# Optimization experiments

Measured on AMD Instinct MI355X. Metric: run time of the kernel, lower is better.

## Reference

```python
import jax, jax.numpy as jnp
import numpy as np

EBIT = 8
BITS = 8  # wl_activate


def block_quantize_global(data, bits):
    """SWALP block quantize, scalar/global path (small_block='None', dim<=4).

    max-abs reduce -> floor(log2) exponent, clamped to signed ebit range ->
    scale -> round-to-nearest-even -> clamp to signed `bits` range -> rescale.
    If max-abs is exactly 0, data is returned unchanged.
    """
    max_entry = jnp.max(jnp.abs(data))
    # guard log2(0); result unused when max_entry == 0
    safe_max = jnp.where(max_entry == 0, jnp.float32(1.0), max_entry)
    max_exponent = jnp.floor(jnp.log2(safe_max))
    emin = -(2.0 ** (EBIT - 1))
    emax = 2.0 ** (EBIT - 1) - 1
    max_exponent = jnp.clip(max_exponent, emin, emax)
    scale = jnp.exp2(-max_exponent + (bits - 2))
    i = jnp.round(data * scale)  # torch.round_ and jnp.round both round half-to-even
    qmin = -(2.0 ** (bits - 1))
    qmax = 2.0 ** (bits - 1) - 1
    i = jnp.clip(i, qmin, qmax)
    out = i * jnp.exp2(max_exponent - (bits - 2))
    return jnp.where(max_entry == 0, data, out)


def setup_inputs() -> dict:
    key = jax.random.key(0)
    x = jax.random.normal(key, (64, 256, 56, 56), dtype=jnp.float32)
    return {"x": x}


def reference(x):
    return block_quantize_global(x, BITS)
```

## Files before the change

### kernel.cpp

```cpp
#include <hip/hip_runtime.h>
#include <math.h>


#define GRID1 2048

typedef float v4f __attribute__((ext_vector_type(4)));

__device__ inline void store_stream(v4f* p, v4f v) {
    asm volatile("global_store_dwordx4 %0, %1, off sc0 sc1 nt" :: "v"(p), "v"(v));
}

__global__ __launch_bounds__(256) void bq_absmax(const float* __restrict__ x,
                                                 float* __restrict__ partial,
                                                 int n) {
    const int n4 = n >> 2;
    const v4f* __restrict__ x4 = (const v4f*)x;
    int tid = blockIdx.x * blockDim.x + threadIdx.x;
    int stride = gridDim.x * blockDim.x;
    float m = 0.0f;
    for (int i = tid; i < n4; i += stride) {
        v4f v = x4[i];
        m = fmaxf(fmaxf(fabsf(v.x), fabsf(v.y)),
                  fmaxf(fmaxf(fabsf(v.z), fabsf(v.w)), m));
    }
    for (int i = (n4 << 2) + tid; i < n; i += stride) m = fmaxf(m, fabsf(x[i]));

    #pragma unroll
    for (int off = 32; off > 0; off >>= 1)
        m = fmaxf(m, __shfl_xor(m, off, 64));

    __shared__ float sm[4];
    if ((threadIdx.x & 63) == 0) sm[threadIdx.x >> 6] = m;
    __syncthreads();
    if (threadIdx.x == 0)
        partial[blockIdx.x] = fmaxf(fmaxf(sm[0], sm[1]), fmaxf(sm[2], sm[3]));
}

__global__ __launch_bounds__(256) void bq_quant(const float* __restrict__ x,
                                                float* __restrict__ out,
                                                const float* __restrict__ partial,
                                                int n) {
    float bm = 0.0f;
    #pragma unroll
    for (int k = 0; k < GRID1 / 256; ++k)
        bm = fmaxf(bm, partial[threadIdx.x + k * 256]);
    #pragma unroll
    for (int off = 32; off > 0; off >>= 1)
        bm = fmaxf(bm, __shfl_xor(bm, off, 64));
    __shared__ float sm[4];
    if ((threadIdx.x & 63) == 0) sm[threadIdx.x >> 6] = bm;
    __syncthreads();
    const float maxe = fmaxf(fmaxf(sm[0], sm[1]), fmaxf(sm[2], sm[3]));

    const int n4 = n >> 2;
    const v4f* __restrict__ x4 = (const v4f*)x;
    v4f* __restrict__ o4 = (v4f*)out;
    const int tid = blockIdx.x * blockDim.x + threadIdx.x;
    const int T = gridDim.x * blockDim.x;
    const int C = (n4 + T - 1) / T;

    if (maxe == 0.0f) {
        for (int c = C - 1; c >= 0; --c) {
            int i = c * T + tid;
            if (i < n4) store_stream(&o4[i], x4[i]);
        }
        for (int i = (n4 << 2) + tid; i < n; i += T) out[i] = x[i];
        return;
    }

    int e = ilogbf(maxe);
    e = max(-128, min(127, e));
    const float scale    = ldexpf(1.0f, -e + 6);
    const float invscale = ldexpf(1.0f, e - 6);

    for (int c = C - 1; c >= 0; --c) {
        int i = c * T + tid;
        if (i < n4) {
            v4f v = x4[i];
            float a = rintf(v.x * scale);
            float b = rintf(v.y * scale);
            float cc = rintf(v.z * scale);
            float d = rintf(v.w * scale);
            a  = fminf(fmaxf(a,  -128.0f), 127.0f);
            b  = fminf(fmaxf(b,  -128.0f), 127.0f);
            cc = fminf(fmaxf(cc, -128.0f), 127.0f);
            d  = fminf(fmaxf(d,  -128.0f), 127.0f);
            v4f r;
            r.x = a * invscale;
            r.y = b * invscale;
            r.z = cc * invscale;
            r.w = d * invscale;
            store_stream(&o4[i], r);
        }
    }
    for (int i = (n4 << 2) + tid; i < n; i += T) {
        float a = rintf(x[i] * scale);
        a = fminf(fmaxf(a, -128.0f), 127.0f);
        out[i] = a * invscale;
    }
}

extern "C" void kernel_launch(void* const* d_in, const int* in_sizes, int n_in,
                              void* d_out, int out_size, void* d_ws, size_t ws_size,
                              hipStream_t stream) {
    const float* x = (const float*)d_in[0];
    float* out = (float*)d_out;
    float* partial = (float*)d_ws;
    int n = in_sizes[0];

    const int block = 256;

    hipLaunchKernelGGL(bq_absmax, dim3(GRID1), dim3(block), 0, stream, x, partial, n);
    hipLaunchKernelGGL(bq_quant,  dim3(GRID1), dim3(block), 0, stream, x, out, partial, n);
}
```

Before: 90.50 us.

## Fuse absmax and quantize into one cooperative kernel with register-resident int8 data

Replaces the two-pass absmax then quantize scheme with one cooperative kernel. Each thread quantizes its chunks on the fly against a running local exponent and packs the int8 values and per-chunk exponents into registers. After a grid sync it rescales those values to the global exponent and writes the output, so the input is read from memory once instead of twice. This relies on a large register array (98 words per thread) and a grid-wide sync. The rescale in the second pass applies a second rounding, which may not match direct rounding exactly in every case.

```diff
diff --git a/kernel.cpp b/kernel.cpp
--- a/kernel.cpp
+++ b/kernel.cpp
@@ -1,7 +1,14 @@
 #include <hip/hip_runtime.h>
+#include <hip/hip_cooperative_groups.h>
 #include <math.h>
 
-
+namespace cg = cooperative_groups;
+
+
+#define NBLK 512
+#define NTHR 256
+#define NTHREADS (NBLK * NTHR)
+#define CHUNKS 98
 #define GRID1 2048
 
 typedef float v4f __attribute__((ext_vector_type(4)));
@@ -9,6 +16,102 @@
 __device__ inline void store_stream(v4f* p, v4f v) {
     asm volatile("global_store_dwordx4 %0, %1, off sc0 sc1 nt" :: "v"(p), "v"(v));
 }
+
+__global__ __launch_bounds__(NTHR, 2) void bq_fused(const float* __restrict__ x,
+                                                    float* __restrict__ out,
+                                                    float* __restrict__ partial) {
+    const int gtid = blockIdx.x * NTHR + threadIdx.x;
+    const v4f* __restrict__ x4 = (const v4f*)x;
+    v4f* __restrict__ o4 = (v4f*)out;
+
+    unsigned int pj[CHUNKS];
+    unsigned int pe[(CHUNKS + 3) / 4];
+
+    float m_run = 0.0f;
+    int   e_run = -32768;
+    float s_run = 0.0f;
+
+    #pragma unroll
+    for (int c = 0; c < CHUNKS; ++c) {
+        const int i4 = c * NTHREADS + gtid;
+        v4f v = x4[i4];
+        float a = fmaxf(fmaxf(fabsf(v.x), fabsf(v.y)),
+                        fmaxf(fabsf(v.z), fabsf(v.w)));
+        if (a > m_run) {
+            m_run = a;
+            int en = ilogbf(a);
+            if (en < -120) en = -120;
+            if (en > e_run) { e_run = en; s_run = ldexpf(1.0f, 6 - e_run); }
+        }
+        int j0 = (int)rintf(v.x * s_run);
+        int j1 = (int)rintf(v.y * s_run);
+        int j2 = (int)rintf(v.z * s_run);
+        int j3 = (int)rintf(v.w * s_run);
+        j0 = min(127, max(-128, j0));
+        j1 = min(127, max(-128, j1));
+        j2 = min(127, max(-128, j2));
+        j3 = min(127, max(-128, j3));
+        pj[c] = (unsigned)(j0 & 0xff)         | ((unsigned)(j1 & 0xff) << 8) |
+                ((unsigned)(j2 & 0xff) << 16) | ((unsigned)(j3 & 0xff) << 24);
+        const unsigned eb = (unsigned)(e_run & 0xff);
+        const int sh = (c & 3) * 8;
+        if ((c & 3) == 0) pe[c >> 2] = eb;
+        else              pe[c >> 2] |= eb << sh;
+    }
+
+    float bm = m_run;
+    #pragma unroll
+    for (int off = 32; off > 0; off >>= 1)
+        bm = fmaxf(bm, __shfl_xor(bm, off, 64));
+    __shared__ float sm[4];
+    if ((threadIdx.x & 63) == 0) sm[threadIdx.x >> 6] = bm;
+    __syncthreads();
+    if (threadIdx.x == 0)
+        partial[blockIdx.x] = fmaxf(fmaxf(sm[0], sm[1]), fmaxf(sm[2], sm[3]));
+
+    cg::this_grid().sync();
+
+    float gm = 0.0f;
+    #pragma unroll
+    for (int k = 0; k < NBLK / NTHR; ++k)
+        gm = fmaxf(gm, partial[threadIdx.x + k * NTHR]);
+    #pragma unroll
+    for (int off = 32; off > 0; off >>= 1)
+        gm = fmaxf(gm, __shfl_xor(gm, off, 64));
+    if ((threadIdx.x & 63) == 0) sm[threadIdx.x >> 6] = gm;
+    __syncthreads();
+    const float maxe = fmaxf(fmaxf(sm[0], sm[1]), fmaxf(sm[2], sm[3]));
+
+    int e_g = 0;
+    if (maxe != 0.0f) {
+        e_g = ilogbf(maxe);
+        e_g = max(-128, min(127, e_g));
+    }
+    const float invs = ldexpf(1.0f, e_g - 6);
+
+    #pragma unroll
+    for (int c = 0; c < CHUNKS; ++c) {
+        const int i4 = c * NTHREADS + gtid;
+        const int ec = (int)(signed char)((pe[c >> 2] >> ((c & 3) * 8)) & 0xffu);
+        const float fs = ldexpf(1.0f, ec - e_g);
+        const unsigned w = pj[c];
+        float f0 = (float)(int)(signed char)(w & 0xff);
+        float f1 = (float)(int)(signed char)((w >> 8) & 0xff);
+        float f2 = (float)(int)(signed char)((w >> 16) & 0xff);
+        float f3 = (float)(int)(signed char)((w >> 24) & 0xff);
+        f0 = fminf(fmaxf(rintf(f0 * fs), -128.0f), 127.0f);
+        f1 = fminf(fmaxf(rintf(f1 * fs), -128.0f), 127.0f);
+        f2 = fminf(fmaxf(rintf(f2 * fs), -128.0f), 127.0f);
+        f3 = fminf(fmaxf(rintf(f3 * fs), -128.0f), 127.0f);
+        v4f r;
+        r.x = f0 * invs;
+        r.y = f1 * invs;
+        r.z = f2 * invs;
+        r.w = f3 * invs;
+        store_stream(&o4[i4], r);
+    }
+}
+
 
 __global__ __launch_bounds__(256) void bq_absmax(const float* __restrict__ x,
                                                  float* __restrict__ partial,
@@ -24,11 +127,9 @@
                   fmaxf(fmaxf(fabsf(v.z), fabsf(v.w)), m));
     }
     for (int i = (n4 << 2) + tid; i < n; i += stride) m = fmaxf(m, fabsf(x[i]));
-
     #pragma unroll
     for (int off = 32; off > 0; off >>= 1)
         m = fmaxf(m, __shfl_xor(m, off, 64));
-
     __shared__ float sm[4];
     if ((threadIdx.x & 63) == 0) sm[threadIdx.x >> 6] = m;
     __syncthreads();
@@ -108,8 +209,26 @@
     float* partial = (float*)d_ws;
     int n = in_sizes[0];
 
-    const int block = 256;
-
-    hipLaunchKernelGGL(bq_absmax, dim3(GRID1), dim3(block), 0, stream, x, partial, n);
-    hipLaunchKernelGGL(bq_quant,  dim3(GRID1), dim3(block), 0, stream, x, out, partial, n);
-}
+    bool coop = (n == NTHREADS * CHUNKS * 4);
+    if (coop) {
+        int nb = 0;
+        if (hipOccupancyMaxActiveBlocksPerMultiprocessor(&nb, (const void*)bq_fused,
+                                                         NTHR, 0) == hipSuccess) {
+            int dev = 0, ncu = 0;
+            hipGetDevice(&dev);
+            hipDeviceGetAttribute(&ncu, hipDeviceAttributeMultiprocessorCount, dev);
+            coop = (nb > 0) && ((long)nb * ncu >= NBLK);
+        } else {
+            coop = false;
+        }
+    }
+    if (coop) {
+        void* args[] = {(void*)&x, (void*)&out, (void*)&partial};
+        coop = hipLaunchCooperativeKernel((const void*)bq_fused, dim3(NBLK),
+                                          dim3(NTHR), args, 0, stream) == hipSuccess;
+    }
+    if (!coop) {
+        hipLaunchKernelGGL(bq_absmax, dim3(GRID1), dim3(256), 0, stream, x, partial, n);
+        hipLaunchKernelGGL(bq_quant,  dim3(GRID1), dim3(256), 0, stream, x, out, partial, n);
+    }
+}
```

Result: no change. 91.42 us (+1.0%).

## Fuse quantization into abs-max pass using per-vector int8 staging

Applied to the files above, without the earlier changes.

Adds a first kernel that computes the abs-max and, in the same pass, quantizes each group of 4 floats to int8 using a local power-of-two exponent. It writes the int8 codes and exponents to the workspace. A second kernel reads this compact form, rescales it to the global exponent, re-rounds and writes the float output. This avoids reading the full float input a second time, at the cost of extra integer math. The double rounding (local then global) can differ from direct round-half-even on some inputs, so correctness is a risk. The old path remains as a fallback, and the quant kernel's loop is simplified to a forward grid stride.

```diff
diff --git a/kernel.cpp b/kernel.cpp
--- a/kernel.cpp
+++ b/kernel.cpp
@@ -9,6 +9,90 @@
 __device__ inline void store_stream(v4f* p, v4f v) {
     asm volatile("global_store_dwordx4 %0, %1, off sc0 sc1 nt" :: "v"(p), "v"(v));
 }
+
+__device__ inline int exp_floor(float m) {
+    int eb = (int)((__float_as_uint(m) >> 23) & 0xff);
+    int e = (eb == 0) ? -120 : eb - 127;
+    return max(-120, min(127, e));
+}
+__device__ inline float exp2i(int k) {
+    return __uint_as_float((unsigned)(k + 127) << 23);
+}
+
+__global__ __launch_bounds__(256) void bq_pack(const float* __restrict__ x,
+                                               unsigned int* __restrict__ j4,
+                                               signed char* __restrict__ e8,
+                                               float* __restrict__ partial,
+                                               int n4) {
+    const v4f* __restrict__ x4 = (const v4f*)x;
+    const int tid = blockIdx.x * blockDim.x + threadIdx.x;
+    const int T = gridDim.x * blockDim.x;
+    float mblk = 0.0f;
+    for (int i = tid; i < n4; i += T) {
+        v4f v = __builtin_nontemporal_load(&x4[i]);
+        float m = fmaxf(fmaxf(fabsf(v.x), fabsf(v.y)),
+                        fmaxf(fabsf(v.z), fabsf(v.w)));
+        mblk = fmaxf(mblk, m);
+        const int e = exp_floor(m);
+        const float s = exp2i(6 - e);
+        int j0 = min(127, max(-128, (int)rintf(v.x * s)));
+        int j1 = min(127, max(-128, (int)rintf(v.y * s)));
+        int j2 = min(127, max(-128, (int)rintf(v.z * s)));
+        int j3 = min(127, max(-128, (int)rintf(v.w * s)));
+        j4[i] = (unsigned)(j0 & 0xff)         | ((unsigned)(j1 & 0xff) << 8) |
+                ((unsigned)(j2 & 0xff) << 16) | ((unsigned)(j3 & 0xff) << 24);
+        e8[i] = (signed char)e;
+    }
+    #pragma unroll
+    for (int off = 32; off > 0; off >>= 1)
+        mblk = fmaxf(mblk, __shfl_xor(mblk, off, 64));
+    __shared__ float sm[4];
+    if ((threadIdx.x & 63) == 0) sm[threadIdx.x >> 6] = mblk;
+    __syncthreads();
+    if (threadIdx.x == 0)
+        partial[blockIdx.x] = fmaxf(fmaxf(sm[0], sm[1]), fmaxf(sm[2], sm[3]));
+}
+
+__global__ __launch_bounds__(256) void bq_emit(const unsigned int* __restrict__ j4,
+                                               const signed char* __restrict__ e8,
+                                               const float* __restrict__ partial,
+                                               float* __restrict__ out,
+                                               int n4) {
+    float gm = 0.0f;
+    #pragma unroll
+    for (int k = 0; k < GRID1 / 256; ++k)
+        gm = fmaxf(gm, partial[threadIdx.x + k * 256]);
+    #pragma unroll
+    for (int off = 32; off > 0; off >>= 1)
+        gm = fmaxf(gm, __shfl_xor(gm, off, 64));
+    __shared__ float sm[4];
+    if ((threadIdx.x & 63) == 0) sm[threadIdx.x >> 6] = gm;
+    __syncthreads();
+    const float maxe = fmaxf(fmaxf(sm[0], sm[1]), fmaxf(sm[2], sm[3]));
+
+    const int eg = exp_floor(maxe);
+    const float invs = exp2i(eg - 6);
+    v4f* __restrict__ o4 = (v4f*)out;
+
+    const int tid = blockIdx.x * blockDim.x + threadIdx.x;
+    const int T = gridDim.x * blockDim.x;
+    for (int i = tid; i < n4; i += T) {
+        const unsigned w = j4[i];
+        const int ec = (int)e8[i];
+        const float fs = ldexpf(1.0f, ec - eg);
+        float f0 = (float)(int)(signed char)(w & 0xff);
+        float f1 = (float)(int)(signed char)((w >> 8) & 0xff);
+        float f2 = (float)(int)(signed char)((w >> 16) & 0xff);
+        float f3 = (float)(int)(signed char)((w >> 24) & 0xff);
+        v4f r;
+        r.x = rintf(f0 * fs) * invs;
+        r.y = rintf(f1 * fs) * invs;
+        r.z = rintf(f2 * fs) * invs;
+        r.w = rintf(f3 * fs) * invs;
+        store_stream(&o4[i], r);
+    }
+}
+
 
 __global__ __launch_bounds__(256) void bq_absmax(const float* __restrict__ x,
                                                  float* __restrict__ partial,
@@ -24,11 +108,9 @@
                   fmaxf(fmaxf(fabsf(v.z), fabsf(v.w)), m));
     }
     for (int i = (n4 << 2) + tid; i < n; i += stride) m = fmaxf(m, fabsf(x[i]));
-
     #pragma unroll
     for (int off = 32; off > 0; off >>= 1)
         m = fmaxf(m, __shfl_xor(m, off, 64));
-
     __shared__ float sm[4];
     if ((threadIdx.x & 63) == 0) sm[threadIdx.x >> 6] = m;
     __syncthreads();
@@ -57,41 +139,32 @@
     v4f* __restrict__ o4 = (v4f*)out;
     const int tid = blockIdx.x * blockDim.x + threadIdx.x;
     const int T = gridDim.x * blockDim.x;
-    const int C = (n4 + T - 1) / T;
 
     if (maxe == 0.0f) {
-        for (int c = C - 1; c >= 0; --c) {
-            int i = c * T + tid;
-            if (i < n4) store_stream(&o4[i], x4[i]);
-        }
+        for (int i = tid; i < n4; i += T) store_stream(&o4[i], x4[i]);
         for (int i = (n4 << 2) + tid; i < n; i += T) out[i] = x[i];
         return;
     }
-
     int e = ilogbf(maxe);
     e = max(-128, min(127, e));
     const float scale    = ldexpf(1.0f, -e + 6);
     const float invscale = ldexpf(1.0f, e - 6);
-
-    for (int c = C - 1; c >= 0; --c) {
-        int i = c * T + tid;
-        if (i < n4) {
-            v4f v = x4[i];
-            float a = rintf(v.x * scale);
-            float b = rintf(v.y * scale);
-            float cc = rintf(v.z * scale);
-            float d = rintf(v.w * scale);
-            a  = fminf(fmaxf(a,  -128.0f), 127.0f);
-            b  = fminf(fmaxf(b,  -128.0f), 127.0f);
-            cc = fminf(fmaxf(cc, -128.0f), 127.0f);
-            d  = fminf(fmaxf(d,  -128.0f), 127.0f);
-            v4f r;
-            r.x = a * invscale;
-            r.y = b * invscale;
-            r.z = cc * invscale;
-            r.w = d * invscale;
-            store_stream(&o4[i], r);
-        }
+    for (int i = tid; i < n4; i += T) {
+        v4f v = x4[i];
+        float a = rintf(v.x * scale);
+        float b = rintf(v.y * scale);
+        float cc = rintf(v.z * scale);
+        float d = rintf(v.w * scale);
+        a  = fminf(fmaxf(a,  -128.0f), 127.0f);
+        b  = fminf(fmaxf(b,  -128.0f), 127.0f);
+        cc = fminf(fmaxf(cc, -128.0f), 127.0f);
+        d  = fminf(fmaxf(d,  -128.0f), 127.0f);
+        v4f r;
+        r.x = a * invscale;
+        r.y = b * invscale;
+        r.z = cc * invscale;
+        r.w = d * invscale;
+        store_stream(&o4[i], r);
     }
     for (int i = (n4 << 2) + tid; i < n; i += T) {
         float a = rintf(x[i] * scale);
@@ -105,11 +178,24 @@
                               hipStream_t stream) {
     const float* x = (const float*)d_in[0];
     float* out = (float*)d_out;
+    int n = in_sizes[0];
+    const int n4 = n >> 2;
+
+    const size_t off_e8 = GRID1 * sizeof(float);
+    const size_t off_j4 = (off_e8 + (size_t)n4 + 15) & ~(size_t)15;
+    const size_t need   = off_j4 + (size_t)n4 * 4;
+
     float* partial = (float*)d_ws;
-    int n = in_sizes[0];
-
-    const int block = 256;
-
-    hipLaunchKernelGGL(bq_absmax, dim3(GRID1), dim3(block), 0, stream, x, partial, n);
-    hipLaunchKernelGGL(bq_quant,  dim3(GRID1), dim3(block), 0, stream, x, out, partial, n);
-}
+
+    if ((n & 3) == 0 && ws_size >= need) {
+        signed char* e8  = (signed char*)d_ws + off_e8;
+        unsigned int* j4 = (unsigned int*)((char*)d_ws + off_j4);
+        hipLaunchKernelGGL(bq_pack, dim3(GRID1), dim3(256), 0, stream,
+                           x, j4, e8, partial, n4);
+        hipLaunchKernelGGL(bq_emit, dim3(GRID1), dim3(256), 0, stream,
+                           j4, e8, partial, out, n4);
+    } else {
+        hipLaunchKernelGGL(bq_absmax, dim3(GRID1), dim3(256), 0, stream, x, partial, n);
+        hipLaunchKernelGGL(bq_quant,  dim3(GRID1), dim3(256), 0, stream, x, out, partial, n);
+    }
+}
```

Measured after the change: 90.26 us. About the same (-0.3%).

## Speculatively quantize per block with local max, fix blocks whose exponent differs

Applied to the files above, without the earlier changes.

Adds a fused path: each block loads its tile into registers, computes a block-local absmax, quantizes with the local exponent, and writes out while recording a partial max. A second kernel reduces the partials to the global exponent and re-quantizes only the blocks whose local exponent differs from the global one. For inputs where most blocks share the global exponent, this avoids the second full read of the input. The path is taken only when n equals a specific size that matches the test shape, and it skips the zero-max special case. It also relies on heavy register use, with 28 float4 values held per thread.

```diff
diff --git a/kernel.cpp b/kernel.cpp
--- a/kernel.cpp
+++ b/kernel.cpp
@@ -2,13 +2,92 @@
 #include <math.h>
 
 
+#define NB 1792
+#define NT 256
+#define CH 28
 #define GRID1 2048
 
 typedef float v4f __attribute__((ext_vector_type(4)));
 
-__device__ inline void store_stream(v4f* p, v4f v) {
-    asm volatile("global_store_dwordx4 %0, %1, off sc0 sc1 nt" :: "v"(p), "v"(v));
+__device__ inline int exp_floor(float m) {
+    int eb = (int)((__float_as_uint(m) >> 23) & 0xff);
+    int e = (eb == 0) ? -120 : eb - 127;
+    return max(-120, min(127, e));
 }
+__device__ inline float exp2i(int k) {
+    return __uint_as_float((unsigned)(k + 127) << 23);
+}
+__device__ inline v4f quant4(v4f v, float s, float inv) {
+    float a = fminf(fmaxf(rintf(v.x * s), -128.0f), 127.0f);
+    float b = fminf(fmaxf(rintf(v.y * s), -128.0f), 127.0f);
+    float c = fminf(fmaxf(rintf(v.z * s), -128.0f), 127.0f);
+    float d = fminf(fmaxf(rintf(v.w * s), -128.0f), 127.0f);
+    v4f r;
+    r.x = a * inv; r.y = b * inv; r.z = c * inv; r.w = d * inv;
+    return r;
+}
+
+__global__ __launch_bounds__(NT) void bq_spec(const float* __restrict__ x,
+                                              float* __restrict__ out,
+                                              float* __restrict__ partial) {
+    const v4f* __restrict__ x4 = (const v4f*)x + (size_t)blockIdx.x * (NT * CH);
+    v4f* __restrict__ o4 = (v4f*)out + (size_t)blockIdx.x * (NT * CH);
+    const int t = threadIdx.x;
+
+    v4f v[CH];
+    #pragma unroll
+    for (int k = 0; k < CH; ++k)
+        v[k] = x4[k * NT + t];
+
+    float m = 0.0f;
+    #pragma unroll
+    for (int k = 0; k < CH; ++k)
+        m = fmaxf(m, fmaxf(fmaxf(fabsf(v[k].x), fabsf(v[k].y)),
+                           fmaxf(fabsf(v[k].z), fabsf(v[k].w))));
+    #pragma unroll
+    for (int off = 32; off > 0; off >>= 1)
+        m = fmaxf(m, __shfl_xor(m, off, 64));
+    __shared__ float sm[4];
+    if ((t & 63) == 0) sm[t >> 6] = m;
+    __syncthreads();
+    const float mb = fmaxf(fmaxf(sm[0], sm[1]), fmaxf(sm[2], sm[3]));
+    if (t == 0) partial[blockIdx.x] = mb;
+
+    const int e = exp_floor(mb);
+    const float s = exp2i(6 - e), inv = exp2i(e - 6);
+    #pragma unroll
+    for (int k = 0; k < CH; ++k)
+        __builtin_nontemporal_store(quant4(v[k], s, inv), &o4[k * NT + t]);
+}
+
+__global__ __launch_bounds__(NT) void bq_fix(const float* __restrict__ x,
+                                             float* __restrict__ out,
+                                             const float* __restrict__ partial) {
+    const int t = threadIdx.x;
+    float g = 0.0f;
+    #pragma unroll
+    for (int k = 0; k < NB / NT; ++k)
+        g = fmaxf(g, partial[t + k * NT]);
+    #pragma unroll
+    for (int off = 32; off > 0; off >>= 1)
+        g = fmaxf(g, __shfl_xor(g, off, 64));
+    __shared__ float sm[4];
+    if ((t & 63) == 0) sm[t >> 6] = g;
+    __syncthreads();
+    const float mg = fmaxf(fmaxf(sm[0], sm[1]), fmaxf(sm[2], sm[3]));
+    const int eg = exp_floor(mg);
+
+    const float mb = partial[blockIdx.x];
+    if (exp_floor(mb) == eg) return;
+
+    const v4f* __restrict__ x4 = (const v4f*)x + (size_t)blockIdx.x * (NT * CH);
+    v4f* __restrict__ o4 = (v4f*)out + (size_t)blockIdx.x * (NT * CH);
+    const float s = exp2i(6 - eg), inv = exp2i(eg - 6);
+    #pragma unroll
+    for (int k = 0; k < CH; ++k)
+        __builtin_nontemporal_store(quant4(x4[k * NT + t], s, inv), &o4[k * NT + t]);
+}
+
 
 __global__ __launch_bounds__(256) void bq_absmax(const float* __restrict__ x,
                                                  float* __restrict__ partial,
@@ -24,11 +103,9 @@
                   fmaxf(fmaxf(fabsf(v.z), fabsf(v.w)), m));
     }
     for (int i = (n4 << 2) + tid; i < n; i += stride) m = fmaxf(m, fabsf(x[i]));
-
     #pragma unroll
     for (int off = 32; off > 0; off >>= 1)
         m = fmaxf(m, __shfl_xor(m, off, 64));
-
     __shared__ float sm[4];
     if ((threadIdx.x & 63) == 0) sm[threadIdx.x >> 6] = m;
     __syncthreads();
@@ -57,42 +134,19 @@
     v4f* __restrict__ o4 = (v4f*)out;
     const int tid = blockIdx.x * blockDim.x + threadIdx.x;
     const int T = gridDim.x * blockDim.x;
-    const int C = (n4 + T - 1) / T;
 
     if (maxe == 0.0f) {
-        for (int c = C - 1; c >= 0; --c) {
-            int i = c * T + tid;
-            if (i < n4) store_stream(&o4[i], x4[i]);
-        }
+        for (int i = tid; i < n4; i += T)
+            __builtin_nontemporal_store(x4[i], &o4[i]);
         for (int i = (n4 << 2) + tid; i < n; i += T) out[i] = x[i];
         return;
     }
-
     int e = ilogbf(maxe);
     e = max(-128, min(127, e));
     const float scale    = ldexpf(1.0f, -e + 6);
     const float invscale = ldexpf(1.0f, e - 6);
-
-    for (int c = C - 1; c >= 0; --c) {
-        int i = c * T + tid;
-        if (i < n4) {
-            v4f v = x4[i];
-            float a = rintf(v.x * scale);
-            float b = rintf(v.y * scale);
-            float cc = rintf(v.z * scale);
-            float d = rintf(v.w * scale);
-            a  = fminf(fmaxf(a,  -128.0f), 127.0f);
-            b  = fminf(fmaxf(b,  -128.0f), 127.0f);
-            cc = fminf(fmaxf(cc, -128.0f), 127.0f);
-            d  = fminf(fmaxf(d,  -128.0f), 127.0f);
-            v4f r;
-            r.x = a * invscale;
-            r.y = b * invscale;
-            r.z = cc * invscale;
-            r.w = d * invscale;
-            store_stream(&o4[i], r);
-        }
-    }
+    for (int i = tid; i < n4; i += T)
+        __builtin_nontemporal_store(quant4(x4[i], scale, invscale), &o4[i]);
     for (int i = (n4 << 2) + tid; i < n; i += T) {
         float a = rintf(x[i] * scale);
         a = fminf(fmaxf(a, -128.0f), 127.0f);
@@ -108,8 +162,12 @@
     float* partial = (float*)d_ws;
     int n = in_sizes[0];
 
-    const int block = 256;
-
-    hipLaunchKernelGGL(bq_absmax, dim3(GRID1), dim3(block), 0, stream, x, partial, n);
-    hipLaunchKernelGGL(bq_quant,  dim3(GRID1), dim3(block), 0, stream, x, out, partial, n);
+    const long need_n = (long)NB * NT * CH * 4;
+    if ((long)n == need_n && ws_size >= (size_t)(GRID1 > NB ? GRID1 : NB) * 4) {
+        hipLaunchKernelGGL(bq_spec, dim3(NB), dim3(NT), 0, stream, x, out, partial);
+        hipLaunchKernelGGL(bq_fix,  dim3(NB), dim3(NT), 0, stream, x, out, partial);
+    } else {
+        hipLaunchKernelGGL(bq_absmax, dim3(GRID1), dim3(256), 0, stream, x, partial, n);
+        hipLaunchKernelGGL(bq_quant,  dim3(GRID1), dim3(256), 0, stream, x, out, partial, n);
+    }
 }
```

New measurement: 76.34 us. 15.6% less time.
